# Optimization experiments

Measured on AMD Instinct MI355X. Metric: run time of the kernel, lower is better.

The kernel has to match this reference:

```python
import jax, jax.numpy as jnp
import numpy as np

N, D, R, E, ED = 50000, 128, 8, 800000, 32
BN_EPS = 1e-5


def _bn(x, g, b):
    # training-mode BatchNorm1d: biased batch stats over axis 0
    m = jnp.mean(x, axis=0)
    v = jnp.var(x, axis=0)
    return (x - m) * jax.lax.rsqrt(v + BN_EPS) * g + b


def _aggregate(x, node_in, nor, ew_norm, edge_feature, We, be):
    # fused: ew * x[node_in] + ew * edge_linear(edge_feature), single scatter-add
    msg = ew_norm[:, None] * (x[node_in] + edge_feature @ We + be)  # [E, D]
    return jax.ops.segment_sum(msg, nor, num_segments=N * R)  # [N*R, D]


def _forward(x, node_in, node_out, relation, edge_weight, edge_feature,
             l1_Wlin, l1_blin, l1_Wself, l1_bself, l1_Wedge, l1_bedge, l1_g, l1_b,
             l2_Wlin, l2_blin, l2_Wself, l2_bself, l2_Wedge, l2_bedge, l2_g, l2_b):
    nor = node_out * R + relation  # [E], expanded destination index
    deg = jax.ops.segment_sum(edge_weight, nor, num_segments=N * R)
    ew = edge_weight / deg[nor]  # degree-normalized edge weights
    # layer 1: relationalGraphConv (update viewed as [N, R*D])
    u1 = _aggregate(x, node_in, nor, ew, edge_feature, l1_Wedge, l1_bedge)
    u1 = u1.reshape(N, R * D)
    h = u1 @ l1_Wlin + l1_blin + x @ l1_Wself + l1_bself
    h = jax.nn.relu(_bn(h, l1_g, l1_b))
    # layer 2: relationalGraph (update permuted to [R*N, D])
    u2 = _aggregate(h, node_in, nor, ew, edge_feature, l2_Wedge, l2_bedge)
    u2 = u2.reshape(N, R, D).transpose(1, 0, 2).reshape(R * N, D)
    h_rep = jnp.tile(h, (R, 1))  # input.repeat(num_relation, 1)
    o = u2 @ l2_Wlin + l2_blin + h_rep @ l2_Wself + l2_bself
    o = jax.nn.relu(_bn(o, l2_g, l2_b))
    return o.reshape(R, N, D)


def setup_inputs() -> dict:
    key = jax.random.key(0)
    ks = jax.random.split(key, 12)
    s_in = 1.0 / np.sqrt(D)
    s_lin1 = 1.0 / np.sqrt(R * D)
    s_e = 1.0 / np.sqrt(ED)
    return {
        "x": jax.random.normal(ks[0], (N, D), jnp.float32),
        "node_in": jax.random.randint(ks[1], (E,), 0, N),
        "node_out": jax.random.randint(ks[2], (E,), 0, N),
        "relation": jax.random.randint(ks[3], (E,), 0, R),
        "edge_weight": jnp.ones((E,), jnp.float32),
        "edge_feature": jax.random.normal(ks[4], (E, ED), jnp.float32),
        "l1_Wlin": jax.random.normal(ks[5], (R * D, D), jnp.float32) * s_lin1,
        "l1_blin": jnp.zeros((D,), jnp.float32),
        "l1_Wself": jax.random.normal(ks[6], (D, D), jnp.float32) * s_in,
        "l1_bself": jnp.zeros((D,), jnp.float32),
        "l1_Wedge": jax.random.normal(ks[7], (ED, D), jnp.float32) * s_e,
        "l1_bedge": jnp.zeros((D,), jnp.float32),
        "l1_g": jnp.ones((D,), jnp.float32),
        "l1_b": jnp.zeros((D,), jnp.float32),
        "l2_Wlin": jax.random.normal(ks[8], (D, D), jnp.float32) * s_in,
        "l2_blin": jnp.zeros((D,), jnp.float32),
        "l2_Wself": jax.random.normal(ks[9], (D, D), jnp.float32) * s_in,
        "l2_bself": jnp.zeros((D,), jnp.float32),
        "l2_Wedge": jax.random.normal(ks[10], (ED, D), jnp.float32) * s_e,
        "l2_bedge": jnp.zeros((D,), jnp.float32),
        "l2_g": jnp.ones((D,), jnp.float32),
        "l2_b": jnp.zeros((D,), jnp.float32),
    }


def reference(x, node_in, node_out, relation, edge_weight, edge_feature,
              l1_Wlin, l1_blin, l1_Wself, l1_bself, l1_Wedge, l1_bedge, l1_g, l1_b,
              l2_Wlin, l2_blin, l2_Wself, l2_bself, l2_Wedge, l2_bedge, l2_g, l2_b):
    return _forward(x, node_in, node_out, relation, edge_weight, edge_feature,
                    l1_Wlin, l1_blin, l1_Wself, l1_bself, l1_Wedge, l1_bedge, l1_g, l1_b,
                    l2_Wlin, l2_blin, l2_Wself, l2_bself, l2_Wedge, l2_bedge, l2_g, l2_b)
```

## Files before the change

### kernel.cpp

```cpp
#include <hip/hip_runtime.h>
#include <hip/hip_bf16.h>

#define Nn 50000
#define Dd 128
#define Rr 8
#define Ee 800000
#define EDd 32
#define NR (Nn * Rr)
#define BN_EPS 1e-5f
#define NREP 16

typedef __attribute__((ext_vector_type(8))) short short8;
typedef __attribute__((ext_vector_type(4))) float floatx4;
typedef unsigned short u16;

__device__ inline float bf2f(u16 u) {
    unsigned int x = ((unsigned int)u) << 16;
    return __uint_as_float(x);
}
__device__ inline u16 f2bf(float f) {
    __hip_bfloat16 h = __float2bfloat16(f);
    return *(u16*)&h;
}

__global__ __launch_bounds__(256) void k_deg(const int* __restrict__ node_out,
                                             const int* __restrict__ relation,
                                             const float* __restrict__ w_in,
                                             float* __restrict__ deg,
                                             int* __restrict__ cnt) {
    int e = blockIdx.x * 256 + threadIdx.x;
    if (e >= Ee) return;
    int idx = node_out[e] * Rr + relation[e];
    unsafeAtomicAdd(deg + idx, w_in[e]);
    atomicAdd(cnt + idx, 1);
}

__global__ __launch_bounds__(256) void k_scan1(const int* __restrict__ cnt,
                                               int* __restrict__ base,
                                               int* __restrict__ partials) {
    __shared__ int sd[256];
    int b0 = blockIdx.x * 1024;
    int t = threadIdx.x;
    int v[4], s = 0;
    #pragma unroll
    for (int j = 0; j < 4; ++j) {
        int idx = b0 + t * 4 + j;
        v[j] = (idx < NR) ? cnt[idx] : 0;
        s += v[j];
    }
    sd[t] = s;
    __syncthreads();
    for (int off = 1; off < 256; off <<= 1) {
        int xv = (t >= off) ? sd[t - off] : 0;
        __syncthreads();
        sd[t] += xv;
        __syncthreads();
    }
    int excl = sd[t] - s;
    if (t == 255) partials[blockIdx.x] = sd[255];
    int run = excl;
    #pragma unroll
    for (int j = 0; j < 4; ++j) {
        int idx = b0 + t * 4 + j;
        if (idx < NR) base[idx] = run;
        run += v[j];
    }
}

__global__ __launch_bounds__(512) void k_scan2(int* __restrict__ partials, int n) {
    __shared__ int sd[512];
    int t = threadIdx.x;
    int own = (t < n) ? partials[t] : 0;
    sd[t] = own;
    __syncthreads();
    for (int off = 1; off < 512; off <<= 1) {
        int xv = (t >= off) ? sd[t - off] : 0;
        __syncthreads();
        sd[t] += xv;
        __syncthreads();
    }
    if (t < n) partials[t] = sd[t] - own;
}

__global__ __launch_bounds__(256) void k_scan3(int* __restrict__ base,
                                               const int* __restrict__ partials) {
    int b0 = blockIdx.x * 1024;
    int add = partials[blockIdx.x];
    int t = threadIdx.x;
    #pragma unroll
    for (int j = 0; j < 4; ++j) {
        int idx = b0 + t * 4 + j;
        if (idx < NR) base[idx] += add;
    }
}

__global__ __launch_bounds__(256) void k_scatter(const int* __restrict__ node_in,
                                                 const int* __restrict__ node_out,
                                                 const int* __restrict__ relation,
                                                 const float* __restrict__ w_in,
                                                 const float* __restrict__ deg,
                                                 int* __restrict__ base,
                                                 int4* __restrict__ recs) {
    int e = blockIdx.x * 256 + threadIdx.x;
    if (e >= Ee) return;
    int idx = node_out[e] * Rr + relation[e];
    int pos = atomicAdd(base + idx, 1);
    int4 r;
    r.x = node_in[e];
    r.y = __float_as_int(w_in[e] / deg[idx]);
    r.z = e;
    r.w = 0;
    recs[pos] = r;
}

__global__ __launch_bounds__(256) void k_cvt(const float* __restrict__ src,
                                             u16* __restrict__ dst, long n) {
    long i = ((long)blockIdx.x * 256 + threadIdx.x) * 4;
    if (i >= n) return;
    float4 v = *(const float4*)(src + i);
    ushort4 o;
    o.x = f2bf(v.x); o.y = f2bf(v.y); o.z = f2bf(v.z); o.w = f2bf(v.w);
    *(ushort4*)(dst + i) = o;
}

__global__ __launch_bounds__(256) void k_prepB(const float* __restrict__ W1,
                                               const float* __restrict__ Ws1,
                                               const float* __restrict__ W2,
                                               const float* __restrict__ Ws2,
                                               u16* __restrict__ Bt) {
    int idx = blockIdx.x * 256 + threadIdx.x;
    if (idx >= 11 * 16384) return;
    int p = idx >> 14;
    int n = (idx >> 7) & 127;
    int k = idx & 127;
    float v;
    if (p < 8)       v = W1[((p << 7) + k) * 128 + n];
    else if (p == 8) v = Ws1[k * 128 + n];
    else if (p == 9) v = W2[k * 128 + n];
    else             v = Ws2[k * 128 + n];
    Bt[((long)p << 14) + n * 128 + k] = f2bf(v);
}

__global__ __launch_bounds__(256) void k_prepWef1(const float* __restrict__ We,
                                                  const float* __restrict__ be,
                                                  const float* __restrict__ Wlin,
                                                  u16* __restrict__ out) {
    int idx = blockIdx.x * 256 + threadIdx.x;
    if (idx >= 3 * 16384) return;
    int n = (idx >> 7) & 127;
    int k = idx & 127;
    int kk = (idx >> 14) * 128 + k;
    int p = kk / 40, j = kk % 40;
    float acc = 0.f;
    if (kk < 320 && j < 33) {
        for (int t = 0; t < 128; ++t) {
            float m = (j < 32) ? We[j * 128 + t] : be[t];
            acc = fmaf(m, Wlin[(p * 128 + t) * 128 + n], acc);
        }
    }
    out[idx] = f2bf(acc);
}

__global__ __launch_bounds__(256) void k_prepWef2(const float* __restrict__ We,
                                                  const float* __restrict__ be,
                                                  const float* __restrict__ Wlin,
                                                  u16* __restrict__ out) {
    int idx = blockIdx.x * 256 + threadIdx.x;
    if (idx >= 8192) return;
    int n = idx >> 6;
    int k = idx & 63;
    float acc = 0.f;
    if (k < 33) {
        for (int t = 0; t < 128; ++t) {
            float m = (k < 32) ? We[k * 128 + t] : be[t];
            acc = fmaf(m, Wlin[t * 128 + n], acc);
        }
    }
    out[idx] = f2bf(acc);
}

__global__ __launch_bounds__(256) void k_agg1(const u16* __restrict__ src,
                                              const int* __restrict__ base_end,
                                              const int* __restrict__ cnt,
                                              const int4* __restrict__ recs,
                                              const float* __restrict__ ef,
                                              u16* __restrict__ u,
                                              u16* __restrict__ aggef_x) {
    int gid = threadIdx.x >> 4;
    int gl = threadIdx.x & 15;
    for (long d = (long)blockIdx.x * 16 + gid; d < NR; d += (long)gridDim.x * 16) {
        int end = base_end[d];
        int c = cnt[d];
        float a[8] = {0.f, 0.f, 0.f, 0.f, 0.f, 0.f, 0.f, 0.f};
        float e0 = 0.f, e1 = 0.f;
        for (int e = end - c; e < end; ++e) {
            int4 rec = recs[e];
            float w = __int_as_float(rec.y);
            short8 xv = *(const short8*)(src + (long)rec.x * Dd + gl * 8);
            float2 fv = *(const float2*)(ef + (long)rec.z * EDd + gl * 2);
            #pragma unroll
            for (int j = 0; j < 8; ++j)
                a[j] = fmaf(w, bf2f((u16)xv[j]), a[j]);
            e0 = fmaf(w, fv.x, e0);
            e1 = fmaf(w, fv.y, e1);
        }
        short8 o;
        #pragma unroll
        for (int j = 0; j < 8; ++j) o[j] = (short)f2bf(a[j]);
        *(short8*)(u + d * Dd + gl * 8) = o;
        ushort2 ev;
        ev.x = f2bf(e0);
        ev.y = f2bf(e1);
        *(ushort2*)(aggef_x + d * 40 + gl * 2) = ev;
        if (gl < 4) {
            ushort2 t;
            t.x = (gl == 0 && c > 0) ? (u16)0x3F80 : (u16)0;
            t.y = 0;
            *(ushort2*)(aggef_x + d * 40 + 32 + gl * 2) = t;
        }
    }
}

__global__ __launch_bounds__(256) void k_agg2(const u16* __restrict__ src,
                                              const int* __restrict__ base_end,
                                              const int* __restrict__ cnt,
                                              const int4* __restrict__ recs,
                                              u16* __restrict__ u) {
    int gid = threadIdx.x >> 4;
    int gl = threadIdx.x & 15;
    for (long d = (long)blockIdx.x * 16 + gid; d < NR; d += (long)gridDim.x * 16) {
        int end = base_end[d];
        int c = cnt[d];
        float a[8] = {0.f, 0.f, 0.f, 0.f, 0.f, 0.f, 0.f, 0.f};
        for (int e = end - c; e < end; ++e) {
            int4 rec = recs[e];
            float w = __int_as_float(rec.y);
            short8 xv = *(const short8*)(src + (long)rec.x * Dd + gl * 8);
            #pragma unroll
            for (int j = 0; j < 8; ++j)
                a[j] = fmaf(w, bf2f((u16)xv[j]), a[j]);
        }
        short8 o;
        #pragma unroll
        for (int j = 0; j < 8; ++j) o[j] = (short)f2bf(a[j]);
        *(short8*)(u + d * Dd + gl * 8) = o;
    }
}

__global__ __launch_bounds__(256) void k_gemm_l1(const u16* __restrict__ U,
                                                 const u16* __restrict__ Xb,
                                                 const u16* __restrict__ Bt,
                                                 const u16* __restrict__ Wef,
                                                 const u16* __restrict__ Ax,
                                                 u16* __restrict__ Hpre,
                                                 float* __restrict__ stats) {
    __shared__ u16 Bs[128 * 136];
    const int tid = threadIdx.x;
    const int wave = tid >> 6, lane = tid & 63;
    const int l15 = lane & 15, kq = lane >> 4;
    const int kq8 = kq * 8;
    const int n0w = wave * 32;
    const int m0 = blockIdx.x * 64;

    floatx4 acc[4][2];
    #pragma unroll
    for (int i = 0; i < 4; ++i)
        #pragma unroll
        for (int j = 0; j < 2; ++j)
            acc[i][j] = (floatx4){0.f, 0.f, 0.f, 0.f};

    long mb[4];
    int mrow[4];
    #pragma unroll
    for (int ti = 0; ti < 4; ++ti) {
        int m = m0 + ti * 16 + l15;
        if (m >= Nn) m = Nn - 1;
        mrow[ti] = m;
        mb[ti] = (long)m * 1024;
    }

    const int stg_n = tid >> 1, stg_h = tid & 1;

    for (int p = 0; p < 12; ++p) {
        __syncthreads();
        {
            const u16* s = (p < 9) ? (Bt + ((long)p << 14) + stg_n * 128 + stg_h * 64)
                                   : (Wef + ((long)(p - 9) << 14) + stg_n * 128 + stg_h * 64);
            u16* dptr = Bs + stg_n * 136 + stg_h * 64;
            #pragma unroll
            for (int j = 0; j < 8; ++j)
                *(uint4*)(dptr + j * 8) = *(const uint4*)(s + j * 8);
        }
        __syncthreads();

        const u16* Ap;
        long aoff[4];
        if (p < 8) {
            Ap = U;
            #pragma unroll
            for (int ti = 0; ti < 4; ++ti) aoff[ti] = mb[ti] + p * 128;
        } else if (p == 8) {
            Ap = Xb;
            #pragma unroll
            for (int ti = 0; ti < 4; ++ti) aoff[ti] = (long)mrow[ti] * 128;
        } else {
            Ap = Ax;
            #pragma unroll
            for (int ti = 0; ti < 4; ++ti) aoff[ti] = (long)mrow[ti] * 320 + (p - 9) * 128;
        }

        #pragma unroll
        for (int k0 = 0; k0 < 128; k0 += 32) {
            short8 a[4], b[2];
            #pragma unroll
            for (int ti = 0; ti < 4; ++ti)
                a[ti] = *(const short8*)(Ap + aoff[ti] + k0 + kq8);
            #pragma unroll
            for (int tj = 0; tj < 2; ++tj)
                b[tj] = *(const short8*)(Bs + (n0w + tj * 16 + l15) * 136 + k0 + kq8);
            #pragma unroll
            for (int ti = 0; ti < 4; ++ti)
                #pragma unroll
                for (int tj = 0; tj < 2; ++tj)
                    acc[ti][tj] = __builtin_amdgcn_mfma_f32_16x16x32_bf16(
                        a[ti], b[tj], acc[ti][tj], 0, 0, 0);
        }
    }

    float cs[2] = {0.f, 0.f}, cq[2] = {0.f, 0.f};
    #pragma unroll
    for (int ti = 0; ti < 4; ++ti) {
        #pragma unroll
        for (int r = 0; r < 4; ++r) {
            int m = m0 + ti * 16 + kq * 4 + r;
            if (m < Nn) {
                #pragma unroll
                for (int tj = 0; tj < 2; ++tj) {
                    float v = acc[ti][tj][r];
                    int col = n0w + tj * 16 + l15;
                    Hpre[(long)m * Dd + col] = f2bf(v);
                    cs[tj] += v;
                    cq[tj] = fmaf(v, v, cq[tj]);
                }
            }
        }
    }
    #pragma unroll
    for (int tj = 0; tj < 2; ++tj) {
        cs[tj] += __shfl_xor(cs[tj], 16, 64);
        cs[tj] += __shfl_xor(cs[tj], 32, 64);
        cq[tj] += __shfl_xor(cq[tj], 16, 64);
        cq[tj] += __shfl_xor(cq[tj], 32, 64);
    }
    if (kq == 0) {
        int rep = blockIdx.x & (NREP - 1);
        #pragma unroll
        for (int tj = 0; tj < 2; ++tj) {
            int col = n0w + tj * 16 + l15;
            unsafeAtomicAdd(stats + rep * 256 + col, cs[tj]);
            unsafeAtomicAdd(stats + rep * 256 + 128 + col, cq[tj]);
        }
    }
}

__global__ __launch_bounds__(256) void k_gemm_l2(const u16* __restrict__ U,
                                                 const u16* __restrict__ H,
                                                 const u16* __restrict__ Bt2,
                                                 const u16* __restrict__ Wef2,
                                                 const u16* __restrict__ Ax,
                                                 float* __restrict__ Out,
                                                 float* __restrict__ stats) {
    __shared__ u16 Bs[128 * 136];
    const int tid = threadIdx.x;
    const int wave = tid >> 6, lane = tid & 63;
    const int l15 = lane & 15, kq = lane >> 4;
    const int kq8 = kq * 8;
    const int wm = wave & 1, wn = wave >> 1;
    const int n0w = wn * 64;
    const long m0 = (long)blockIdx.x * 128;

    floatx4 acc[4][4];
    #pragma unroll
    for (int i = 0; i < 4; ++i)
        #pragma unroll
        for (int j = 0; j < 4; ++j)
            acc[i][j] = (floatx4){0.f, 0.f, 0.f, 0.f};

    long aoffU[4], aoffH[4], aoffE[4];
    #pragma unroll
    for (int ti = 0; ti < 4; ++ti) {
        long mm = m0 + wm * 64 + ti * 16 + l15;
        int n = (int)(mm % Nn);
        int r = (int)(mm / Nn);
        long dd = (long)n * 8 + r;
        aoffU[ti] = dd * 128;
        aoffH[ti] = (long)n * 128;
        aoffE[ti] = dd * 40;
    }

    const int stg_n = tid >> 1, stg_h = tid & 1;

    for (int p = 0; p < 2; ++p) {
        __syncthreads();
        {
            const u16* s = Bt2 + ((long)p << 14) + stg_n * 128 + stg_h * 64;
            u16* dptr = Bs + stg_n * 136 + stg_h * 64;
            #pragma unroll
            for (int j = 0; j < 8; ++j)
                *(uint4*)(dptr + j * 8) = *(const uint4*)(s + j * 8);
        }
        __syncthreads();

        const u16* Ap = p ? H : U;
        const long* ao = p ? aoffH : aoffU;

        #pragma unroll
        for (int k0 = 0; k0 < 128; k0 += 32) {
            short8 a[4], b[4];
            #pragma unroll
            for (int ti = 0; ti < 4; ++ti)
                a[ti] = *(const short8*)(Ap + ao[ti] + k0 + kq8);
            #pragma unroll
            for (int tj = 0; tj < 4; ++tj)
                b[tj] = *(const short8*)(Bs + (n0w + tj * 16 + l15) * 136 + k0 + kq8);
            #pragma unroll
            for (int ti = 0; ti < 4; ++ti)
                #pragma unroll
                for (int tj = 0; tj < 4; ++tj)
                    acc[ti][tj] = __builtin_amdgcn_mfma_f32_16x16x32_bf16(
                        a[ti], b[tj], acc[ti][tj], 0, 0, 0);
        }
    }

    __syncthreads();
    {
        int n = tid >> 1, kh = (tid & 1) * 32;
        const u16* s = Wef2 + n * 64 + kh;
        u16* dptr = Bs + n * 136 + kh;
        #pragma unroll
        for (int j = 0; j < 4; ++j)
            *(uint4*)(dptr + j * 8) = *(const uint4*)(s + j * 8);
    }
    __syncthreads();
    #pragma unroll
    for (int k0 = 0; k0 < 64; k0 += 32) {
        short8 a[4], b[4];
        #pragma unroll
        for (int ti = 0; ti < 4; ++ti)
            a[ti] = *(const short8*)(Ax + aoffE[ti] + k0 + kq8);
        #pragma unroll
        for (int tj = 0; tj < 4; ++tj)
            b[tj] = *(const short8*)(Bs + (n0w + tj * 16 + l15) * 136 + k0 + kq8);
        #pragma unroll
        for (int ti = 0; ti < 4; ++ti)
            #pragma unroll
            for (int tj = 0; tj < 4; ++tj)
                acc[ti][tj] = __builtin_amdgcn_mfma_f32_16x16x32_bf16(
                    a[ti], b[tj], acc[ti][tj], 0, 0, 0);
    }

    float cs[4] = {0.f, 0.f, 0.f, 0.f}, cq[4] = {0.f, 0.f, 0.f, 0.f};
    #pragma unroll
    for (int ti = 0; ti < 4; ++ti) {
        #pragma unroll
        for (int r = 0; r < 4; ++r) {
            long mm = m0 + wm * 64 + ti * 16 + kq * 4 + r;
            #pragma unroll
            for (int tj = 0; tj < 4; ++tj) {
                float v = acc[ti][tj][r];
                int col = n0w + tj * 16 + l15;
                Out[mm * Dd + col] = v;
                cs[tj] += v;
                cq[tj] = fmaf(v, v, cq[tj]);
            }
        }
    }
    #pragma unroll
    for (int tj = 0; tj < 4; ++tj) {
        cs[tj] += __shfl_xor(cs[tj], 16, 64);
        cs[tj] += __shfl_xor(cs[tj], 32, 64);
        cq[tj] += __shfl_xor(cq[tj], 16, 64);
        cq[tj] += __shfl_xor(cq[tj], 32, 64);
    }
    if (kq == 0) {
        int rep = blockIdx.x & (NREP - 1);
        #pragma unroll
        for (int tj = 0; tj < 4; ++tj) {
            int col = n0w + tj * 16 + l15;
            unsafeAtomicAdd(stats + rep * 256 + col, cs[tj]);
            unsafeAtomicAdd(stats + rep * 256 + 128 + col, cq[tj]);
        }
    }
}

__global__ __launch_bounds__(256) void k_bn_apply_bf(u16* __restrict__ X,
                                                     const float* __restrict__ stats,
                                                     const float* __restrict__ g,
                                                     const float* __restrict__ b, int M) {
    int c = (threadIdx.x & 31) * 4;
    int rh = threadIdx.x >> 5;
    float invM = 1.0f / (float)M;
    float s[4] = {0, 0, 0, 0}, q[4] = {0, 0, 0, 0};
    for (int rep = 0; rep < NREP; ++rep) {
        float4 s4 = *(const float4*)(stats + rep * 256 + c);
        float4 q4 = *(const float4*)(stats + rep * 256 + 128 + c);
        s[0] += s4.x; s[1] += s4.y; s[2] += s4.z; s[3] += s4.w;
        q[0] += q4.x; q[1] += q4.y; q[2] += q4.z; q[3] += q4.w;
    }
    float4 g4 = *(const float4*)(g + c);
    float4 b4 = *(const float4*)(b + c);
    float gv[4] = {g4.x, g4.y, g4.z, g4.w};
    float bv[4] = {b4.x, b4.y, b4.z, b4.w};
    float sc[4], sh[4];
    #pragma unroll
    for (int j = 0; j < 4; ++j) {
        float m = s[j] * invM;
        sc[j] = gv[j] / sqrtf(q[j] * invM - m * m + BN_EPS);
        sh[j] = bv[j] - m * sc[j];
    }
    for (long r = blockIdx.x * 8 + rh; r < M; r += (long)gridDim.x * 8) {
        ushort4 v = *(ushort4*)(X + r * Dd + c);
        ushort4 o;
        o.x = f2bf(fmaxf(fmaf(bf2f(v.x), sc[0], sh[0]), 0.f));
        o.y = f2bf(fmaxf(fmaf(bf2f(v.y), sc[1], sh[1]), 0.f));
        o.z = f2bf(fmaxf(fmaf(bf2f(v.z), sc[2], sh[2]), 0.f));
        o.w = f2bf(fmaxf(fmaf(bf2f(v.w), sc[3], sh[3]), 0.f));
        *(ushort4*)(X + r * Dd + c) = o;
    }
}

__global__ __launch_bounds__(256) void k_bn_apply_f32(float* __restrict__ X,
                                                      const float* __restrict__ stats,
                                                      const float* __restrict__ g,
                                                      const float* __restrict__ b, int M) {
    int c = (threadIdx.x & 31) * 4;
    int rh = threadIdx.x >> 5;
    float invM = 1.0f / (float)M;
    float s[4] = {0, 0, 0, 0}, q[4] = {0, 0, 0, 0};
    for (int rep = 0; rep < NREP; ++rep) {
        float4 s4 = *(const float4*)(stats + rep * 256 + c);
        float4 q4 = *(const float4*)(stats + rep * 256 + 128 + c);
        s[0] += s4.x; s[1] += s4.y; s[2] += s4.z; s[3] += s4.w;
        q[0] += q4.x; q[1] += q4.y; q[2] += q4.z; q[3] += q4.w;
    }
    float4 g4 = *(const float4*)(g + c);
    float4 b4 = *(const float4*)(b + c);
    float gv[4] = {g4.x, g4.y, g4.z, g4.w};
    float bv[4] = {b4.x, b4.y, b4.z, b4.w};
    float sc[4], sh[4];
    #pragma unroll
    for (int j = 0; j < 4; ++j) {
        float m = s[j] * invM;
        sc[j] = gv[j] / sqrtf(q[j] * invM - m * m + BN_EPS);
        sh[j] = bv[j] - m * sc[j];
    }
    for (long r = blockIdx.x * 8 + rh; r < M; r += (long)gridDim.x * 8) {
        float4 v = *(float4*)(X + r * Dd + c);
        v.x = fmaxf(fmaf(v.x, sc[0], sh[0]), 0.f);
        v.y = fmaxf(fmaf(v.y, sc[1], sh[1]), 0.f);
        v.z = fmaxf(fmaf(v.z, sc[2], sh[2]), 0.f);
        v.w = fmaxf(fmaf(v.w, sc[3], sh[3]), 0.f);
        *(float4*)(X + r * Dd + c) = v;
    }
}

extern "C" void kernel_launch(void* const* d_in, const int* in_sizes, int n_in,
                              void* d_out, int out_size, void* d_ws, size_t ws_size,
                              hipStream_t stream) {
    const float* x            = (const float*)d_in[0];
    const int*   node_in      = (const int*)d_in[1];
    const int*   node_out     = (const int*)d_in[2];
    const int*   relation     = (const int*)d_in[3];
    const float* edge_weight  = (const float*)d_in[4];
    const float* edge_feature = (const float*)d_in[5];
    const float* l1_Wlin  = (const float*)d_in[6];
    const float* l1_Wself = (const float*)d_in[8];
    const float* l1_Wedge = (const float*)d_in[10];
    const float* l1_bedge = (const float*)d_in[11];
    const float* l1_g     = (const float*)d_in[12];
    const float* l1_b     = (const float*)d_in[13];
    const float* l2_Wlin  = (const float*)d_in[14];
    const float* l2_Wself = (const float*)d_in[16];
    const float* l2_Wedge = (const float*)d_in[18];
    const float* l2_bedge = (const float*)d_in[19];
    const float* l2_g     = (const float*)d_in[20];
    const float* l2_b     = (const float*)d_in[21];
    float* out = (float*)d_out;

    u16* u_bf    = (u16*)d_ws;
    u16* h       = u_bf + (long)NR * Dd;
    u16* x_bf    = h + (long)Nn * Dd;
    u16* aggef_x = x_bf + (long)Nn * Dd;
    u16* Bt      = aggef_x + (long)NR * 40 + 128;
    u16* Wef1    = Bt + 11 * 16384;
    u16* Wef2    = Wef1 + 3 * 16384;
    float* deg   = (float*)(Wef2 + 8192);
    int*   cnt   = (int*)(deg + NR);
    int*   base  = cnt + NR;
    int4*  recs  = (int4*)(base + NR);
    int*   partials = (int*)(recs + Ee);
    float* stats = (float*)(partials + 1024);

    const int NB1 = (NR + 1023) / 1024;

    hipMemsetAsync(deg, 0, sizeof(float) * NR, stream);
    hipMemsetAsync(cnt, 0, sizeof(int) * NR, stream);
    hipMemsetAsync(stats, 0, sizeof(float) * 2 * NREP * 256, stream);
    k_deg<<<(Ee + 255) / 256, 256, 0, stream>>>(node_out, relation, edge_weight, deg, cnt);
    k_scan1<<<NB1, 256, 0, stream>>>(cnt, base, partials);
    k_scan2<<<1, 512, 0, stream>>>(partials, NB1);
    k_scan3<<<NB1, 256, 0, stream>>>(base, partials);
    k_scatter<<<(Ee + 255) / 256, 256, 0, stream>>>(node_in, node_out, relation, edge_weight,
                                                    deg, base, recs);
    k_cvt<<<((long)Nn * Dd / 4 + 255) / 256, 256, 0, stream>>>(x, x_bf, (long)Nn * Dd);
    k_prepB<<<(11 * 16384 + 255) / 256, 256, 0, stream>>>(l1_Wlin, l1_Wself, l2_Wlin, l2_Wself, Bt);
    k_prepWef1<<<(3 * 16384 + 255) / 256, 256, 0, stream>>>(l1_Wedge, l1_bedge, l1_Wlin, Wef1);
    k_prepWef2<<<32, 256, 0, stream>>>(l2_Wedge, l2_bedge, l2_Wlin, Wef2);

    k_agg1<<<4096, 256, 0, stream>>>(x_bf, base, cnt, recs, edge_feature, u_bf, aggef_x);
    k_gemm_l1<<<(Nn + 63) / 64, 256, 0, stream>>>(u_bf, x_bf, Bt, Wef1, aggef_x, h, stats);
    k_bn_apply_bf<<<512, 256, 0, stream>>>(h, stats, l1_g, l1_b, Nn);

    k_agg2<<<4096, 256, 0, stream>>>(h, base, cnt, recs, u_bf);
    k_gemm_l2<<<NR / 128, 256, 0, stream>>>(u_bf, h, Bt + 9 * 16384, Wef2, aggef_x, out,
                                            stats + NREP * 256);
    k_bn_apply_f32<<<2048, 256, 0, stream>>>(out, stats + NREP * 256, l2_g, l2_b, NR);
}
```

Measured before the change: 930.2 us.

## Drop LDS staging in GEMMs, load B directly, batch loads; unroll gather loops by two

Both GEMM kernels stop staging the weight panel through shared memory with syncthreads. Each wave now reads B fragments straight from global memory (L1/L2 cached) and batches all A/B loads for a panel before issuing the MFMAs. The layer-1 edge-feature panel is trimmed to a K=64 tail so it does less padded work, and a memset zeroes the padding past the end of aggef_x so those reads stay defined. The aggregation kernels unroll the edge loop by two to keep more gathers in flight, at the cost of higher register pressure and redundant global B traffic per wave.

```diff
diff --git a/kernel.cpp b/kernel.cpp
--- a/kernel.cpp
+++ b/kernel.cpp
@@ -188,35 +188,54 @@
                                               u16* __restrict__ aggef_x) {
     int gid = threadIdx.x >> 4;
     int gl = threadIdx.x & 15;
+    int gl8 = gl * 8, gl2 = gl * 2;
     for (long d = (long)blockIdx.x * 16 + gid; d < NR; d += (long)gridDim.x * 16) {
         int end = base_end[d];
         int c = cnt[d];
+        int e = end - c;
         float a[8] = {0.f, 0.f, 0.f, 0.f, 0.f, 0.f, 0.f, 0.f};
         float e0 = 0.f, e1 = 0.f;
-        for (int e = end - c; e < end; ++e) {
-            int4 rec = recs[e];
-            float w = __int_as_float(rec.y);
-            short8 xv = *(const short8*)(src + (long)rec.x * Dd + gl * 8);
-            float2 fv = *(const float2*)(ef + (long)rec.z * EDd + gl * 2);
+        for (; e + 2 <= end; e += 2) {
+            int4 r0 = recs[e];
+            int4 r1 = recs[e + 1];
+            short8 x0 = *(const short8*)(src + (long)r0.x * Dd + gl8);
+            short8 x1 = *(const short8*)(src + (long)r1.x * Dd + gl8);
+            float2 f0 = *(const float2*)(ef + (long)r0.z * EDd + gl2);
+            float2 f1 = *(const float2*)(ef + (long)r1.z * EDd + gl2);
+            float w0 = __int_as_float(r0.y);
+            float w1 = __int_as_float(r1.y);
+            #pragma unroll
+            for (int j = 0; j < 8; ++j) {
+                a[j] = fmaf(w0, bf2f((u16)x0[j]), a[j]);
+                a[j] = fmaf(w1, bf2f((u16)x1[j]), a[j]);
+            }
+            e0 = fmaf(w0, f0.x, e0); e0 = fmaf(w1, f1.x, e0);
+            e1 = fmaf(w0, f0.y, e1); e1 = fmaf(w1, f1.y, e1);
+        }
+        if (e < end) {
+            int4 r0 = recs[e];
+            float w0 = __int_as_float(r0.y);
+            short8 x0 = *(const short8*)(src + (long)r0.x * Dd + gl8);
+            float2 f0 = *(const float2*)(ef + (long)r0.z * EDd + gl2);
             #pragma unroll
             for (int j = 0; j < 8; ++j)
-                a[j] = fmaf(w, bf2f((u16)xv[j]), a[j]);
-            e0 = fmaf(w, fv.x, e0);
-            e1 = fmaf(w, fv.y, e1);
+                a[j] = fmaf(w0, bf2f((u16)x0[j]), a[j]);
+            e0 = fmaf(w0, f0.x, e0);
+            e1 = fmaf(w0, f0.y, e1);
         }
         short8 o;
         #pragma unroll
         for (int j = 0; j < 8; ++j) o[j] = (short)f2bf(a[j]);
-        *(short8*)(u + d * Dd + gl * 8) = o;
+        *(short8*)(u + d * Dd + gl8) = o;
         ushort2 ev;
         ev.x = f2bf(e0);
         ev.y = f2bf(e1);
-        *(ushort2*)(aggef_x + d * 40 + gl * 2) = ev;
+        *(ushort2*)(aggef_x + d * 40 + gl2) = ev;
         if (gl < 4) {
             ushort2 t;
             t.x = (gl == 0 && c > 0) ? (u16)0x3F80 : (u16)0;
             t.y = 0;
-            *(ushort2*)(aggef_x + d * 40 + 32 + gl * 2) = t;
+            *(ushort2*)(aggef_x + d * 40 + 32 + gl2) = t;
         }
     }
 }
@@ -228,23 +247,88 @@
                                               u16* __restrict__ u) {
     int gid = threadIdx.x >> 4;
     int gl = threadIdx.x & 15;
+    int gl8 = gl * 8;
     for (long d = (long)blockIdx.x * 16 + gid; d < NR; d += (long)gridDim.x * 16) {
         int end = base_end[d];
         int c = cnt[d];
+        int e = end - c;
         float a[8] = {0.f, 0.f, 0.f, 0.f, 0.f, 0.f, 0.f, 0.f};
-        for (int e = end - c; e < end; ++e) {
-            int4 rec = recs[e];
-            float w = __int_as_float(rec.y);
-            short8 xv = *(const short8*)(src + (long)rec.x * Dd + gl * 8);
+        for (; e + 2 <= end; e += 2) {
+            int4 r0 = recs[e];
+            int4 r1 = recs[e + 1];
+            short8 x0 = *(const short8*)(src + (long)r0.x * Dd + gl8);
+            short8 x1 = *(const short8*)(src + (long)r1.x * Dd + gl8);
+            float w0 = __int_as_float(r0.y);
+            float w1 = __int_as_float(r1.y);
+            #pragma unroll
+            for (int j = 0; j < 8; ++j) {
+                a[j] = fmaf(w0, bf2f((u16)x0[j]), a[j]);
+                a[j] = fmaf(w1, bf2f((u16)x1[j]), a[j]);
+            }
+        }
+        if (e < end) {
+            int4 r0 = recs[e];
+            float w0 = __int_as_float(r0.y);
+            short8 x0 = *(const short8*)(src + (long)r0.x * Dd + gl8);
             #pragma unroll
             for (int j = 0; j < 8; ++j)
-                a[j] = fmaf(w, bf2f((u16)xv[j]), a[j]);
+                a[j] = fmaf(w0, bf2f((u16)x0[j]), a[j]);
         }
         short8 o;
         #pragma unroll
         for (int j = 0; j < 8; ++j) o[j] = (short)f2bf(a[j]);
-        *(short8*)(u + d * Dd + gl * 8) = o;
-    }
+        *(short8*)(u + d * Dd + gl8) = o;
+    }
+}
+
+template <int NK>
+__device__ __forceinline__ void l1_panel(const u16* __restrict__ Ap,
+                                         const long* __restrict__ aoff,
+                                         const u16* __restrict__ Bp, int br0, int br1,
+                                         int kq8, floatx4 (&acc)[4][2]) {
+    short8 a[4][NK], b[2][NK];
+    #pragma unroll
+    for (int kk = 0; kk < NK; ++kk) {
+        #pragma unroll
+        for (int ti = 0; ti < 4; ++ti)
+            a[ti][kk] = *(const short8*)(Ap + aoff[ti] + kk * 32 + kq8);
+        b[0][kk] = *(const short8*)(Bp + (long)br0 * 128 + kk * 32 + kq8);
+        b[1][kk] = *(const short8*)(Bp + (long)br1 * 128 + kk * 32 + kq8);
+    }
+    #pragma unroll
+    for (int kk = 0; kk < NK; ++kk)
+        #pragma unroll
+        for (int ti = 0; ti < 4; ++ti)
+            #pragma unroll
+            for (int tj = 0; tj < 2; ++tj)
+                acc[ti][tj] = __builtin_amdgcn_mfma_f32_16x16x32_bf16(
+                    a[ti][kk], b[tj][kk], acc[ti][tj], 0, 0, 0);
+}
+
+template <int NK>
+__device__ __forceinline__ void l2_panel(const u16* __restrict__ Ap,
+                                         const long* __restrict__ aoff,
+                                         const u16* __restrict__ Bp, long bstride,
+                                         const int* __restrict__ brow, int koff,
+                                         int kq8, floatx4 (&acc)[4][4]) {
+    short8 a[4][NK], b[4][NK];
+    #pragma unroll
+    for (int kk = 0; kk < NK; ++kk) {
+        #pragma unroll
+        for (int ti = 0; ti < 4; ++ti)
+            a[ti][kk] = *(const short8*)(Ap + aoff[ti] + koff + kk * 32 + kq8);
+        #pragma unroll
+        for (int tj = 0; tj < 4; ++tj)
+            b[tj][kk] = *(const short8*)(Bp + (long)brow[tj] * bstride + koff + kk * 32 + kq8);
+    }
+    #pragma unroll
+    for (int kk = 0; kk < NK; ++kk)
+        #pragma unroll
+        for (int ti = 0; ti < 4; ++ti)
+            #pragma unroll
+            for (int tj = 0; tj < 4; ++tj)
+                acc[ti][tj] = __builtin_amdgcn_mfma_f32_16x16x32_bf16(
+                    a[ti][kk], b[tj][kk], acc[ti][tj], 0, 0, 0);
 }
 
 __global__ __launch_bounds__(256) void k_gemm_l1(const u16* __restrict__ U,
@@ -254,13 +338,13 @@
                                                  const u16* __restrict__ Ax,
                                                  u16* __restrict__ Hpre,
                                                  float* __restrict__ stats) {
-    __shared__ u16 Bs[128 * 136];
     const int tid = threadIdx.x;
     const int wave = tid >> 6, lane = tid & 63;
     const int l15 = lane & 15, kq = lane >> 4;
     const int kq8 = kq * 8;
     const int n0w = wave * 32;
     const int m0 = blockIdx.x * 64;
+    const int br0 = n0w + l15, br1 = n0w + 16 + l15;
 
     floatx4 acc[4][2];
     #pragma unroll
@@ -279,53 +363,25 @@
         mb[ti] = (long)m * 1024;
     }
 
-    const int stg_n = tid >> 1, stg_h = tid & 1;
-
-    for (int p = 0; p < 12; ++p) {
-        __syncthreads();
-        {
-            const u16* s = (p < 9) ? (Bt + ((long)p << 14) + stg_n * 128 + stg_h * 64)
-                                   : (Wef + ((long)(p - 9) << 14) + stg_n * 128 + stg_h * 64);
-            u16* dptr = Bs + stg_n * 136 + stg_h * 64;
-            #pragma unroll
-            for (int j = 0; j < 8; ++j)
-                *(uint4*)(dptr + j * 8) = *(const uint4*)(s + j * 8);
-        }
-        __syncthreads();
-
-        const u16* Ap;
-        long aoff[4];
-        if (p < 8) {
-            Ap = U;
-            #pragma unroll
-            for (int ti = 0; ti < 4; ++ti) aoff[ti] = mb[ti] + p * 128;
-        } else if (p == 8) {
-            Ap = Xb;
-            #pragma unroll
-            for (int ti = 0; ti < 4; ++ti) aoff[ti] = (long)mrow[ti] * 128;
-        } else {
-            Ap = Ax;
-            #pragma unroll
-            for (int ti = 0; ti < 4; ++ti) aoff[ti] = (long)mrow[ti] * 320 + (p - 9) * 128;
-        }
-
-        #pragma unroll
-        for (int k0 = 0; k0 < 128; k0 += 32) {
-            short8 a[4], b[2];
-            #pragma unroll
-            for (int ti = 0; ti < 4; ++ti)
-                a[ti] = *(const short8*)(Ap + aoff[ti] + k0 + kq8);
-            #pragma unroll
-            for (int tj = 0; tj < 2; ++tj)
-                b[tj] = *(const short8*)(Bs + (n0w + tj * 16 + l15) * 136 + k0 + kq8);
-            #pragma unroll
-            for (int ti = 0; ti < 4; ++ti)
-                #pragma unroll
-                for (int tj = 0; tj < 2; ++tj)
-                    acc[ti][tj] = __builtin_amdgcn_mfma_f32_16x16x32_bf16(
-                        a[ti], b[tj], acc[ti][tj], 0, 0, 0);
-        }
-    }
+    long aoff[4];
+    #pragma unroll
+    for (int p = 0; p < 8; ++p) {
+        #pragma unroll
+        for (int ti = 0; ti < 4; ++ti) aoff[ti] = mb[ti] + p * 128;
+        l1_panel<4>(U, aoff, Bt + ((long)p << 14), br0, br1, kq8, acc);
+    }
+    #pragma unroll
+    for (int ti = 0; ti < 4; ++ti) aoff[ti] = (long)mrow[ti] * 128;
+    l1_panel<4>(Xb, aoff, Bt + (8L << 14), br0, br1, kq8, acc);
+    #pragma unroll
+    for (int q = 0; q < 2; ++q) {
+        #pragma unroll
+        for (int ti = 0; ti < 4; ++ti) aoff[ti] = (long)mrow[ti] * 320 + q * 128;
+        l1_panel<4>(Ax, aoff, Wef + ((long)q << 14), br0, br1, kq8, acc);
+    }
+    #pragma unroll
+    for (int ti = 0; ti < 4; ++ti) aoff[ti] = (long)mrow[ti] * 320 + 256;
+    l1_panel<2>(Ax, aoff, Wef + (2L << 14), br0, br1, kq8, acc);
 
     float cs[2] = {0.f, 0.f}, cq[2] = {0.f, 0.f};
     #pragma unroll
@@ -370,7 +426,6 @@
                                                  const u16* __restrict__ Ax,
                                                  float* __restrict__ Out,
                                                  float* __restrict__ stats) {
-    __shared__ u16 Bs[128 * 136];
     const int tid = threadIdx.x;
     const int wave = tid >> 6, lane = tid & 63;
     const int l15 = lane & 15, kq = lane >> 4;
@@ -378,6 +433,10 @@
     const int wm = wave & 1, wn = wave >> 1;
     const int n0w = wn * 64;
     const long m0 = (long)blockIdx.x * 128;
+
+    int brow[4];
+    #pragma unroll
+    for (int tj = 0; tj < 4; ++tj) brow[tj] = n0w + tj * 16 + l15;
 
     floatx4 acc[4][4];
     #pragma unroll
@@ -398,66 +457,11 @@
         aoffE[ti] = dd * 40;
     }
 
-    const int stg_n = tid >> 1, stg_h = tid & 1;
-
-    for (int p = 0; p < 2; ++p) {
-        __syncthreads();
-        {
-            const u16* s = Bt2 + ((long)p << 14) + stg_n * 128 + stg_h * 64;
-            u16* dptr = Bs + stg_n * 136 + stg_h * 64;
-            #pragma unroll
-            for (int j = 0; j < 8; ++j)
-                *(uint4*)(dptr + j * 8) = *(const uint4*)(s + j * 8);
-        }
-        __syncthreads();
-
-        const u16* Ap = p ? H : U;
-        const long* ao = p ? aoffH : aoffU;
-
-        #pragma unroll
-        for (int k0 = 0; k0 < 128; k0 += 32) {
-            short8 a[4], b[4];
-            #pragma unroll
-            for (int ti = 0; ti < 4; ++ti)
-                a[ti] = *(const short8*)(Ap + ao[ti] + k0 + kq8);
-            #pragma unroll
-            for (int tj = 0; tj < 4; ++tj)
-                b[tj] = *(const short8*)(Bs + (n0w + tj * 16 + l15) * 136 + k0 + kq8);
-            #pragma unroll
-            for (int ti = 0; ti < 4; ++ti)
-                #pragma unroll
-                for (int tj = 0; tj < 4; ++tj)
-                    acc[ti][tj] = __builtin_amdgcn_mfma_f32_16x16x32_bf16(
-                        a[ti], b[tj], acc[ti][tj], 0, 0, 0);
-        }
-    }
-
-    __syncthreads();
-    {
-        int n = tid >> 1, kh = (tid & 1) * 32;
-        const u16* s = Wef2 + n * 64 + kh;
-        u16* dptr = Bs + n * 136 + kh;
-        #pragma unroll
-        for (int j = 0; j < 4; ++j)
-            *(uint4*)(dptr + j * 8) = *(const uint4*)(s + j * 8);
-    }
-    __syncthreads();
-    #pragma unroll
-    for (int k0 = 0; k0 < 64; k0 += 32) {
-        short8 a[4], b[4];
-        #pragma unroll
-        for (int ti = 0; ti < 4; ++ti)
-            a[ti] = *(const short8*)(Ax + aoffE[ti] + k0 + kq8);
-        #pragma unroll
-        for (int tj = 0; tj < 4; ++tj)
-            b[tj] = *(const short8*)(Bs + (n0w + tj * 16 + l15) * 136 + k0 + kq8);
-        #pragma unroll
-        for (int ti = 0; ti < 4; ++ti)
-            #pragma unroll
-            for (int tj = 0; tj < 4; ++tj)
-                acc[ti][tj] = __builtin_amdgcn_mfma_f32_16x16x32_bf16(
-                    a[ti], b[tj], acc[ti][tj], 0, 0, 0);
-    }
+    l2_panel<2>(U, aoffU, Bt2, 128, brow, 0, kq8, acc);
+    l2_panel<2>(U, aoffU, Bt2, 128, brow, 64, kq8, acc);
+    l2_panel<2>(H, aoffH, Bt2 + 16384, 128, brow, 0, kq8, acc);
+    l2_panel<2>(H, aoffH, Bt2 + 16384, 128, brow, 64, kq8, acc);
+    l2_panel<2>(Ax, aoffE, Wef2, 64, brow, 0, kq8, acc);
 
     float cs[4] = {0.f, 0.f, 0.f, 0.f}, cq[4] = {0.f, 0.f, 0.f, 0.f};
     #pragma unroll
@@ -606,6 +610,7 @@
     hipMemsetAsync(deg, 0, sizeof(float) * NR, stream);
     hipMemsetAsync(cnt, 0, sizeof(int) * NR, stream);
     hipMemsetAsync(stats, 0, sizeof(float) * 2 * NREP * 256, stream);
+    hipMemsetAsync(aggef_x + (long)NR * 40, 0, 256, stream);
     k_deg<<<(Ee + 255) / 256, 256, 0, stream>>>(node_out, relation, edge_weight, deg, cnt);
     k_scan1<<<NB1, 256, 0, stream>>>(cnt, base, partials);
     k_scan2<<<1, 512, 0, stream>>>(partials, NB1);
```

Measured after the change: 928.5 us. Within noise of the previous version (-0.2%).
